# Performance work log

Hardware: AMD Instinct MI355X
Metric: run time of the kernel (lower is better)

Reference implementation:

```python
import jax, jax.numpy as jnp
import numpy as np

NUM_HEADS = 12


def setup_inputs() -> dict:
    key = jax.random.key(0)
    k1, k2, k3 = jax.random.split(key, 3)
    B, N, C = 2, 2048, 768
    x = jax.random.normal(k1, (B, N, C), dtype=jnp.float32)
    w_qkv = jax.random.normal(k2, (C, 3 * C), dtype=jnp.float32) * 0.02
    w_proj = jax.random.normal(k3, (C, C), dtype=jnp.float32) * 0.02
    b_proj = jnp.zeros((C,), dtype=jnp.float32)
    return {"x": x, "w_qkv": w_qkv, "w_proj": w_proj, "b_proj": b_proj}


def reference(x, w_qkv, w_proj, b_proj):
    B, N, C = x.shape
    H = NUM_HEADS
    D = C // H
    qkv = (x @ w_qkv).reshape(B, N, 3, H, D)  # [B,N,3,H,D]
    q = jnp.transpose(qkv[:, :, 0], (0, 2, 1, 3))  # [B,H,N,D]
    k = jnp.transpose(qkv[:, :, 1], (0, 2, 1, 3))
    v = jnp.transpose(qkv[:, :, 2], (0, 2, 1, 3))
    # ELU+1 feature map (note: self.scale is unused in the original forward)
    q = jax.nn.elu(q) + 1.0
    k = jax.nn.elu(k) + 1.0
    attn = jnp.einsum("bhnd,bhmd->bhnm", q, k)  # explicit O(N^2) as in source
    attn = attn / jnp.sum(attn, axis=-1, keepdims=True)
    out = jnp.einsum("bhnm,bhmd->bhnd", attn, v)  # [B,H,N,D]
    out = jnp.transpose(out, (0, 2, 1, 3)).reshape(B, N, C)
    out = out @ w_proj + b_proj
    return out, attn
```

## Files before the change

### kernel.cpp

```cpp
#include <hip/hip_runtime.h>
#include <hip/hip_bf16.h>
#include <cstdint>
#include <cmath>

#define BDIM 256

constexpr int Bb = 2;
constexpr int Nn = 2048;
constexpr int Cc = 768;
constexpr int Hh = 12;
constexpr int Dd = 64;
constexpr int TC = 3 * Cc;
constexpr int BH = Bb * Hh;
constexpr int NCHUNK = 16;
constexpr int CHROWS = Nn / NCHUNK;

typedef __attribute__((ext_vector_type(8))) short short8v;
typedef __attribute__((ext_vector_type(4))) float f32x4;

__device__ __forceinline__ float elu1(float x) {
  return x > 0.f ? x + 1.f : expf(x);
}

__device__ __forceinline__ unsigned short f2bf(float f) {
  uint32_t u = __float_as_uint(f);
  uint32_t r = (u + 0x7fff + ((u >> 16) & 1)) >> 16;
  return (unsigned short)r;
}
__device__ __forceinline__ float bf2f(unsigned short h) {
  return __uint_as_float(((uint32_t)h) << 16);
}

__device__ __forceinline__ void gll16(const unsigned short* g, unsigned short* ldsbase) {
  __builtin_amdgcn_global_load_lds((const __attribute__((address_space(1))) void*)g,
                                   (__attribute__((address_space(3))) void*)ldsbase,
                                   16, 0, 0);
}

constexpr int XBLK = 3072;
constexpr int WQBLK = (TC / 32) * (Cc / 32);
constexpr int WPBLK = (Cc / 32) * (Cc / 32);

__device__ __forceinline__ void castT_tile(const float* __restrict__ W,
                                           unsigned short* __restrict__ Wh,
                                           int K, int N, int n0, int k0, int tid,
                                           float (*t)[33]) {
  const int r = tid >> 3, c4 = (tid & 7) * 4;
  float4 v = *(const float4*)&W[(size_t)(k0 + r) * N + n0 + c4];
  t[r][c4 + 0] = v.x;
  t[r][c4 + 1] = v.y;
  t[r][c4 + 2] = v.z;
  t[r][c4 + 3] = v.w;
  __syncthreads();
  const int n = tid >> 3, k4 = (tid & 7) * 4;
  ushort4 h;
  h.x = f2bf(t[k4 + 0][n]);
  h.y = f2bf(t[k4 + 1][n]);
  h.z = f2bf(t[k4 + 2][n]);
  h.w = f2bf(t[k4 + 3][n]);
  *(ushort4*)&Wh[(size_t)(n0 + n) * K + k0 + k4] = h;
}

__global__ __launch_bounds__(BDIM) void fused_cast(const float* __restrict__ x,
                                                   const float* __restrict__ w_qkv,
                                                   const float* __restrict__ w_proj,
                                                   unsigned short* __restrict__ xh,
                                                   unsigned short* __restrict__ wqh,
                                                   unsigned short* __restrict__ wph) {
  __shared__ float t[32][33];
  const int bid = blockIdx.x, tid = threadIdx.x;
  if (bid < XBLK) {
    int i = (bid * BDIM + tid) * 4;
    float4 v = *(const float4*)&x[i];
    ushort4 h;
    h.x = f2bf(v.x);
    h.y = f2bf(v.y);
    h.z = f2bf(v.z);
    h.w = f2bf(v.w);
    *(ushort4*)&xh[i] = h;
  } else if (bid < XBLK + WQBLK) {
    int q = bid - XBLK;
    castT_tile(w_qkv, wqh, Cc, TC, (q % (TC / 32)) * 32, (q / (TC / 32)) * 32, tid, t);
  } else {
    int p = bid - XBLK - WQBLK;
    castT_tile(w_proj, wph, Cc, Cc, (p % (Cc / 32)) * 32, (p / (Cc / 32)) * 32, tid, t);
  }
}

template <int EP>
__device__ __forceinline__ void mfma_core(
    int bx, int by, int bz,
    const unsigned short* __restrict__ A, const unsigned short* __restrict__ Bt,
    const float* __restrict__ bias, const float* __restrict__ denom,
    float* __restrict__ C, int Mrows, int Nw, int K,
    long sAz, long sBz, long sCz,
    unsigned short* __restrict__ qpb, unsigned short* __restrict__ kpb,
    unsigned short* __restrict__ vpb,
    unsigned short* lds, float* dnls) {
  const unsigned short* A0 = A + (size_t)bz * sAz;
  const unsigned short* B0 = Bt + (size_t)bz * sBz;
  float* Cz = C + (size_t)bz * sCz;

  const int tid = threadIdx.x;
  const int wave = tid >> 6, lane = tid & 63;
  const int wr = wave >> 1, wc = wave & 1;
  const int row0 = by * 128, col0 = bx * 128;
  const int l15 = lane & 15, l4 = lane >> 4;
  const int srow = wave * 16 + (lane >> 2);
  const int scol = (lane & 3) * 8;
  const int wbase = wave * 512;

  float dnv_reg = 0.f;
  if constexpr (EP == 1) dnv_reg = denom[(size_t)bz * Mrows + row0 + (tid & 127)];

  auto STAGE = [&](int buf, int k0) {
    unsigned short* dst = lds + buf * 8192 + wbase;
    gll16(&A0[(size_t)(row0 + srow) * K + k0 + scol], dst);
    gll16(&A0[(size_t)(row0 + 64 + srow) * K + k0 + scol], dst + 2048);
    gll16(&B0[(size_t)(col0 + srow) * K + k0 + scol], dst + 4096);
    gll16(&B0[(size_t)(col0 + 64 + srow) * K + k0 + scol], dst + 6144);
  };

  f32x4 acc[4][4];
#pragma unroll
  for (int i = 0; i < 4; ++i)
#pragma unroll
    for (int j = 0; j < 4; ++j) acc[i][j] = {0.f, 0.f, 0.f, 0.f};

  auto COMPUTE = [&](int buf) {
    const unsigned short* la = lds + buf * 8192;
    const unsigned short* lb = la + 4096;
    short8v av[4], bv[4];
#pragma unroll
    for (int i = 0; i < 4; ++i)
      av[i] = *(const short8v*)&la[(wr * 64 + i * 16 + l15) * 32 + l4 * 8];
#pragma unroll
    for (int j = 0; j < 4; ++j)
      bv[j] = *(const short8v*)&lb[(wc * 64 + j * 16 + l15) * 32 + l4 * 8];
#pragma unroll
    for (int i = 0; i < 4; ++i)
#pragma unroll
      for (int j = 0; j < 4; ++j)
        acc[i][j] = __builtin_amdgcn_mfma_f32_16x16x32_bf16(av[i], bv[j], acc[i][j], 0, 0, 0);
  };

  const int nt = K >> 5;
  STAGE(0, 0);
  if (nt > 1) STAGE(1, 32);
  int cur = 0;
  for (int t = 0; t < nt; ++t) {
    if (t < nt - 1)
      asm volatile("s_waitcnt vmcnt(4)" ::: "memory");
    else
      asm volatile("s_waitcnt vmcnt(0)" ::: "memory");
    __builtin_amdgcn_s_barrier();
    COMPUTE(cur);
    if (t < nt - 2) {
      __builtin_amdgcn_s_barrier();
      STAGE(cur, (t + 2) * 32);
    }
    cur ^= 1;
  }

  if constexpr (EP == 0) {
#pragma unroll
    for (int i = 0; i < 4; ++i) {
      const int rbase = row0 + wr * 64 + i * 16 + l4 * 4;
#pragma unroll
      for (int j = 0; j < 4; ++j) {
        const int col = col0 + wc * 64 + j * 16 + l15;
        float bs = bias[col];
#pragma unroll
        for (int r = 0; r < 4; ++r)
          __builtin_nontemporal_store(acc[i][j][r] + bs,
                                      &Cz[(size_t)(rbase + r) * Nw + col]);
      }
    }
  } else if constexpr (EP == 1) {
    if (tid < 128) dnls[tid] = 1.0f / dnv_reg;
    float* fl = (float*)lds;
#pragma unroll
    for (int i = 0; i < 4; ++i) {
      __syncthreads();
#pragma unroll
      for (int j = 0; j < 4; ++j)
#pragma unroll
        for (int r = 0; r < 4; ++r)
          fl[(wr * 16 + l4 * 4 + r) * 132 + wc * 64 + j * 16 + l15] =
              acc[i][j][r] * dnls[wr * 64 + i * 16 + l4 * 4 + r];
      __syncthreads();
#pragma unroll
      for (int p = 0; p < 4; ++p) {
        int f4 = p * 256 + tid;
        int cr = f4 >> 5, c4 = (f4 & 31) * 4;
        f32x4 v = *(const f32x4*)&fl[cr * 132 + c4];
        int grow = row0 + (cr >> 4) * 64 + i * 16 + (cr & 15);
        __builtin_nontemporal_store(v, (f32x4*)&Cz[(size_t)grow * Nw + col0 + c4]);
      }
    }
  } else {
    const int tt = bx / 6;
    const int rcbase = (bx % 6) * 128 + wc * 64;
#pragma unroll
    for (int i = 0; i < 4; ++i) {
      const int rowb = row0 + wr * 64 + i * 16 + l4 * 4;
#pragma unroll
      for (int j = 0; j < 4; ++j) {
        const int rc = rcbase + j * 16 + l15;
        const int h = rc >> 6, d = rc & 63;
#pragma unroll
        for (int r = 0; r < 4; ++r) {
          const int row = rowb + r;
          const int b = row >> 11, n = row & (Nn - 1);
          const size_t idx = ((size_t)(b * Hh + h) * Nn + n) * 64 + d;
          float val = acc[i][j][r];
          if (tt == 0) {
            qpb[idx] = f2bf(elu1(val));
          } else if (tt == 1) {
            kpb[idx] = f2bf(elu1(val));
          } else {
            vpb[idx] = f2bf(val);
          }
        }
      }
    }
  }
}

__global__ __launch_bounds__(BDIM) void gemm_qkv_k(
    const unsigned short* __restrict__ xh, const unsigned short* __restrict__ wqh,
    unsigned short* __restrict__ qpb, unsigned short* __restrict__ kpb,
    unsigned short* __restrict__ vpb) {
  __shared__ __align__(16) unsigned short lds[16384];
  __shared__ float dnls[128];
  const int bid = blockIdx.x;
  const int swz = (bid & 7) * 72 + (bid >> 3);
  const int bx = swz % 18, by = swz / 18;
  mfma_core<2>(bx, by, 0, xh, wqh, nullptr, nullptr, nullptr, Bb * Nn, TC, Cc,
               0, 0, 0, qpb, kpb, vpb, lds, dnls);
}

__global__ __launch_bounds__(BDIM) void attn_proj_k(
    const unsigned short* __restrict__ qpb, const unsigned short* __restrict__ kpb,
    const float* __restrict__ denom, float* __restrict__ attn,
    const unsigned short* __restrict__ oph, const unsigned short* __restrict__ wph,
    const float* __restrict__ b_proj, float* __restrict__ out) {
  __shared__ __align__(16) unsigned short lds[16384];
  __shared__ float dnls[128];
  const int bid = blockIdx.x;
  if (bid < 6144) {
    const int swz = (bid & 7) * 768 + (bid >> 3);
    const int bz = swz >> 8, rem = swz & 255;
    const int by = rem >> 4, bx = rem & 15;
    mfma_core<1>(bx, by, bz, qpb, kpb, nullptr, denom, attn, Nn, Nn, Dd,
                 (long)Nn * Dd, (long)Nn * Dd, (long)Nn * Nn,
                 nullptr, nullptr, nullptr, lds, dnls);
  } else {
    const int p = bid - 6144;
    mfma_core<0>(p % 6, p / 6, 0, oph, wph, b_proj, nullptr, out, Bb * Nn, Cc, Cc,
                 0, 0, 0, nullptr, nullptr, nullptr, lds, dnls);
  }
}

__global__ __launch_bounds__(BDIM) void kv_partial(const unsigned short* __restrict__ kpb,
                                                   const unsigned short* __restrict__ vpb,
                                                   float* __restrict__ kvpart,
                                                   float* __restrict__ kspart) {
  const int chunk = blockIdx.x, bh = blockIdx.y;
  __shared__ unsigned short ks[16][64];
  __shared__ unsigned short vs[16][64];
  __shared__ float ksl[16][64];
  const int tid = threadIdx.x;
  const int e = tid & 63, dg = tid >> 6;
  const int srow = tid >> 4, sd4 = (tid & 15) * 4;
  float acc[16] = {};
  float ksp[4] = {0.f, 0.f, 0.f, 0.f};
  const int n0base = chunk * CHROWS;
  for (int s = 0; s < CHROWS; s += 16) {
    const int n = n0base + s + srow;
    ushort4 kk = *(const ushort4*)&kpb[((size_t)bh * Nn + n) * 64 + sd4];
    ushort4 vv = *(const ushort4*)&vpb[((size_t)bh * Nn + n) * 64 + sd4];
    __syncthreads();
    *(ushort4*)&ks[srow][sd4] = kk;
    *(ushort4*)&vs[srow][sd4] = vv;
    ksp[0] += bf2f(kk.x);
    ksp[1] += bf2f(kk.y);
    ksp[2] += bf2f(kk.z);
    ksp[3] += bf2f(kk.w);
    __syncthreads();
#pragma unroll
    for (int j = 0; j < 16; ++j) {
      const float v = bf2f(vs[j][e]);
      short8v k8a = *(const short8v*)&ks[j][dg * 16];
      short8v k8b = *(const short8v*)&ks[j][dg * 16 + 8];
#pragma unroll
      for (int d = 0; d < 8; ++d) acc[d] += bf2f((unsigned short)k8a[d]) * v;
#pragma unroll
      for (int d = 0; d < 8; ++d) acc[8 + d] += bf2f((unsigned short)k8b[d]) * v;
    }
  }
  float* outp = kvpart + (size_t)(bh * NCHUNK + chunk) * 4096;
#pragma unroll
  for (int d = 0; d < 16; ++d) outp[(dg * 16 + d) * 64 + e] = acc[d];
  ksl[srow][sd4 + 0] = ksp[0];
  ksl[srow][sd4 + 1] = ksp[1];
  ksl[srow][sd4 + 2] = ksp[2];
  ksl[srow][sd4 + 3] = ksp[3];
  __syncthreads();
  if (tid < 64) {
    float s2 = 0.f;
#pragma unroll
    for (int r = 0; r < 16; ++r) s2 += ksl[r][tid];
    kspart[(bh * NCHUNK + chunk) * 64 + tid] = s2;
  }
}

__global__ __launch_bounds__(BDIM) void kv_reduce(const float* __restrict__ kvpart,
                                                  const float* __restrict__ kspart,
                                                  unsigned short* __restrict__ kvtb,
                                                  float* __restrict__ ksum) {
  const int seg = blockIdx.x, bh = blockIdx.y, tid = threadIdx.x;
  const int idx = seg * 256 + tid;
  float s = 0.f;
#pragma unroll 4
  for (int c = 0; c < NCHUNK; ++c) s += kvpart[(size_t)(bh * NCHUNK + c) * 4096 + idx];
  const int dk = idx >> 6, dv = idx & 63;
  kvtb[(size_t)bh * 4096 + dv * 64 + dk] = f2bf(s);
  if (tid < 4) {
    int e = seg * 4 + tid;
    float s2 = 0.f;
#pragma unroll 4
    for (int c = 0; c < NCHUNK; ++c) s2 += kspart[(bh * NCHUNK + c) * 64 + e];
    ksum[bh * 64 + e] = s2;
  }
}

__global__ __launch_bounds__(BDIM) void outpre_mfma(
    const unsigned short* __restrict__ qpb, const unsigned short* __restrict__ kvtb,
    const float* __restrict__ ksum, float* __restrict__ denom,
    unsigned short* __restrict__ oph) {
  const int nc = blockIdx.x, bh = blockIdx.y;
  const int b = bh / Hh, h = bh % Hh;
  __shared__ float kss[64];
  __shared__ float dnls[128];
  const int tid = threadIdx.x;
  const int wv = tid >> 6, lane = tid & 63;
  const int l15 = lane & 15, l4 = lane >> 4;
  if (tid < 64) kss[tid] = ksum[bh * 64 + tid];

  const int rowb = nc * 128 + wv * 32;
  const unsigned short* Aq = qpb + ((size_t)bh * Nn + rowb) * 64;
  const unsigned short* Bk = kvtb + (size_t)bh * 4096;

  short8v av[2][2], bv[4][2];
#pragma unroll
  for (int ks = 0; ks < 2; ++ks) {
#pragma unroll
    for (int i = 0; i < 2; ++i)
      av[i][ks] = *(const short8v*)&Aq[(size_t)(i * 16 + l15) * 64 + ks * 32 + l4 * 8];
#pragma unroll
    for (int j = 0; j < 4; ++j)
      bv[j][ks] = *(const short8v*)&Bk[(size_t)(j * 16 + l15) * 64 + ks * 32 + l4 * 8];
  }
  f32x4 acc[2][4];
#pragma unroll
  for (int i = 0; i < 2; ++i)
#pragma unroll
    for (int j = 0; j < 4; ++j) acc[i][j] = {0.f, 0.f, 0.f, 0.f};
#pragma unroll
  for (int ks = 0; ks < 2; ++ks)
#pragma unroll
    for (int i = 0; i < 2; ++i)
#pragma unroll
      for (int j = 0; j < 4; ++j)
        acc[i][j] = __builtin_amdgcn_mfma_f32_16x16x32_bf16(av[i][ks], bv[j][ks],
                                                            acc[i][j], 0, 0, 0);

  __syncthreads();
  float dpart[2] = {0.f, 0.f};
#pragma unroll
  for (int ks = 0; ks < 2; ++ks)
#pragma unroll
    for (int i = 0; i < 2; ++i)
#pragma unroll
      for (int t = 0; t < 8; ++t)
        dpart[i] += bf2f((unsigned short)av[i][ks][t]) * kss[ks * 32 + l4 * 8 + t];
#pragma unroll
  for (int i = 0; i < 2; ++i) {
    dpart[i] += __shfl_xor(dpart[i], 16);
    dpart[i] += __shfl_xor(dpart[i], 32);
    if (l4 == 0) {
      dnls[wv * 32 + i * 16 + l15] = dpart[i];
      denom[(size_t)bh * Nn + rowb + i * 16 + l15] = dpart[i];
    }
  }
  __syncthreads();
#pragma unroll
  for (int i = 0; i < 2; ++i) {
#pragma unroll
    for (int r = 0; r < 4; ++r) {
      const int rl = i * 16 + l4 * 4 + r;
      const float rd = 1.0f / dnls[wv * 32 + rl];
      const int nrow = rowb + rl;
#pragma unroll
      for (int j = 0; j < 4; ++j)
        oph[((size_t)b * Nn + nrow) * Cc + h * 64 + j * 16 + l15] =
            f2bf(acc[i][j][r] * rd);
    }
  }
}

extern "C" void kernel_launch(void* const* d_in, const int* in_sizes, int n_in,
                              void* d_out, int out_size, void* d_ws, size_t ws_size,
                              hipStream_t stream) {
  const float* x = (const float*)d_in[0];
  const float* w_qkv = (const float*)d_in[1];
  const float* w_proj = (const float*)d_in[2];
  const float* b_proj = (const float*)d_in[3];
  float* out = (float*)d_out;
  float* attn = out + (size_t)Bb * Nn * Cc;

  float* ws = (float*)d_ws;
  float* kvpart = ws;
  float* kspart = kvpart + 1572864;
  float* ksum = kspart + 24576;
  float* denom = ksum + 2048;
  unsigned short* us = (unsigned short*)(denom + 49152);
  unsigned short* xh = us;
  unsigned short* wqh = xh + 3145728;
  unsigned short* qpb = wqh + 1769472;
  unsigned short* kpb = qpb + 3145728;
  unsigned short* vpb = kpb + 3145728;
  unsigned short* kvtb = vpb + 3145728;
  unsigned short* oph = kvtb + 98304;
  unsigned short* wph = oph + 3145728;

  fused_cast<<<dim3(XBLK + WQBLK + WPBLK), BDIM, 0, stream>>>(x, w_qkv, w_proj, xh, wqh,
                                                              wph);
  gemm_qkv_k<<<dim3(576), BDIM, 0, stream>>>(xh, wqh, qpb, kpb, vpb);
  kv_partial<<<dim3(NCHUNK, BH), BDIM, 0, stream>>>(kpb, vpb, kvpart, kspart);
  kv_reduce<<<dim3(16, BH), BDIM, 0, stream>>>(kvpart, kspart, kvtb, ksum);
  outpre_mfma<<<dim3(Nn / 128, BH), BDIM, 0, stream>>>(qpb, kvtb, ksum, denom, oph);
  attn_proj_k<<<dim3(6144 + 192), BDIM, 0, stream>>>(qpb, kpb, denom, attn,
                                                     oph, wph, b_proj, out);
}
```

Before: 149.7 us.

## Compute two attention column tiles per block with overlapped K prefetch

The attention-matrix kernel now computes a 128x256 output region per block as two 128-column tiles. It reuses the Q fragments held in registers and prefetches the second K tile while the first tile's epilogue writes out. The row denominator is recomputed in-kernel from ksum as a dot product with Q, so the denom array is no longer read. This halves the block count and cuts redundant Q loads, at the cost of more LDS per block and possibly lower occupancy.

```diff
diff --git a/kernel.cpp b/kernel.cpp
--- a/kernel.cpp
+++ b/kernel.cpp
@@ -91,12 +91,12 @@
 __device__ __forceinline__ void mfma_core(
     int bx, int by, int bz,
     const unsigned short* __restrict__ A, const unsigned short* __restrict__ Bt,
-    const float* __restrict__ bias, const float* __restrict__ denom,
+    const float* __restrict__ bias,
     float* __restrict__ C, int Mrows, int Nw, int K,
     long sAz, long sBz, long sCz,
     unsigned short* __restrict__ qpb, unsigned short* __restrict__ kpb,
     unsigned short* __restrict__ vpb,
-    unsigned short* lds, float* dnls) {
+    unsigned short* lds) {
   const unsigned short* A0 = A + (size_t)bz * sAz;
   const unsigned short* B0 = Bt + (size_t)bz * sBz;
   float* Cz = C + (size_t)bz * sCz;
@@ -109,9 +109,6 @@
   const int srow = wave * 16 + (lane >> 2);
   const int scol = (lane & 3) * 8;
   const int wbase = wave * 512;
-
-  float dnv_reg = 0.f;
-  if constexpr (EP == 1) dnv_reg = denom[(size_t)bz * Mrows + row0 + (tid & 127)];
 
   auto STAGE = [&](int buf, int k0) {
     unsigned short* dst = lds + buf * 8192 + wbase;
@@ -176,28 +173,6 @@
                                       &Cz[(size_t)(rbase + r) * Nw + col]);
       }
     }
-  } else if constexpr (EP == 1) {
-    if (tid < 128) dnls[tid] = 1.0f / dnv_reg;
-    float* fl = (float*)lds;
-#pragma unroll
-    for (int i = 0; i < 4; ++i) {
-      __syncthreads();
-#pragma unroll
-      for (int j = 0; j < 4; ++j)
-#pragma unroll
-        for (int r = 0; r < 4; ++r)
-          fl[(wr * 16 + l4 * 4 + r) * 132 + wc * 64 + j * 16 + l15] =
-              acc[i][j][r] * dnls[wr * 64 + i * 16 + l4 * 4 + r];
-      __syncthreads();
-#pragma unroll
-      for (int p = 0; p < 4; ++p) {
-        int f4 = p * 256 + tid;
-        int cr = f4 >> 5, c4 = (f4 & 31) * 4;
-        f32x4 v = *(const f32x4*)&fl[cr * 132 + c4];
-        int grow = row0 + (cr >> 4) * 64 + i * 16 + (cr & 15);
-        __builtin_nontemporal_store(v, (f32x4*)&Cz[(size_t)grow * Nw + col0 + c4]);
-      }
-    }
   } else {
     const int tt = bx / 6;
     const int rcbase = (bx % 6) * 128 + wc * 64;
@@ -232,34 +207,143 @@
     unsigned short* __restrict__ qpb, unsigned short* __restrict__ kpb,
     unsigned short* __restrict__ vpb) {
   __shared__ __align__(16) unsigned short lds[16384];
-  __shared__ float dnls[128];
   const int bid = blockIdx.x;
   const int swz = (bid & 7) * 72 + (bid >> 3);
   const int bx = swz % 18, by = swz / 18;
-  mfma_core<2>(bx, by, 0, xh, wqh, nullptr, nullptr, nullptr, Bb * Nn, TC, Cc,
-               0, 0, 0, qpb, kpb, vpb, lds, dnls);
+  mfma_core<2>(bx, by, 0, xh, wqh, nullptr, nullptr, Bb * Nn, TC, Cc,
+               0, 0, 0, qpb, kpb, vpb, lds);
 }
 
 __global__ __launch_bounds__(BDIM) void attn_proj_k(
     const unsigned short* __restrict__ qpb, const unsigned short* __restrict__ kpb,
-    const float* __restrict__ denom, float* __restrict__ attn,
+    const float* __restrict__ ksum, float* __restrict__ attn,
     const unsigned short* __restrict__ oph, const unsigned short* __restrict__ wph,
     const float* __restrict__ b_proj, float* __restrict__ out) {
-  __shared__ __align__(16) unsigned short lds[16384];
+  __shared__ __align__(16) unsigned short lds[24832];
+  __shared__ float kss[64];
   __shared__ float dnls[128];
-  const int bid = blockIdx.x;
-  if (bid < 6144) {
-    const int swz = (bid & 7) * 768 + (bid >> 3);
-    const int bz = swz >> 8, rem = swz & 255;
-    const int by = rem >> 4, bx = rem & 15;
-    mfma_core<1>(bx, by, bz, qpb, kpb, nullptr, denom, attn, Nn, Nn, Dd,
-                 (long)Nn * Dd, (long)Nn * Dd, (long)Nn * Nn,
-                 nullptr, nullptr, nullptr, lds, dnls);
-  } else {
-    const int p = bid - 6144;
-    mfma_core<0>(p % 6, p / 6, 0, oph, wph, b_proj, nullptr, out, Bb * Nn, Cc, Cc,
-                 0, 0, 0, nullptr, nullptr, nullptr, lds, dnls);
-  }
+  const int bid = blockIdx.x, tid = threadIdx.x;
+  if (bid >= 3072) {
+    const int p = bid - 3072;
+    mfma_core<0>(p % 6, p / 6, 0, oph, wph, b_proj, out, Bb * Nn, Cc, Cc,
+                 0, 0, 0, nullptr, nullptr, nullptr, lds);
+    return;
+  }
+  const int swz = (bid & 7) * 384 + (bid >> 3);
+  const int bz = swz >> 7, rem = swz & 127;
+  const int by = rem >> 3, bxp = rem & 7;
+  const int row0 = by * 128, col00 = bxp * 256;
+  const int wave = tid >> 6, lane = tid & 63;
+  const int wr = wave >> 1, wc = wave & 1;
+  const int l15 = lane & 15, l4 = lane >> 4;
+  const int srow = wave * 16 + (lane >> 2);
+  const int scol = (lane & 3) * 8;
+  const int wbase = wave * 512;
+  const unsigned short* Aq = qpb + (size_t)bz * Nn * 64;
+  const unsigned short* Bk = kpb + (size_t)bz * Nn * 64;
+  float* Cz = attn + (size_t)bz * Nn * Nn;
+  float* fl = (float*)(lds + 16384);
+
+  if (tid < 64) kss[tid] = ksum[bz * 64 + tid];
+
+  gll16(&Aq[(size_t)(row0 + srow) * 64 + scol], lds + wbase);
+  gll16(&Aq[(size_t)(row0 + 64 + srow) * 64 + scol], lds + 2048 + wbase);
+  gll16(&Aq[(size_t)(row0 + srow) * 64 + 32 + scol], lds + 4096 + wbase);
+  gll16(&Aq[(size_t)(row0 + 64 + srow) * 64 + 32 + scol], lds + 4096 + 2048 + wbase);
+  gll16(&Bk[(size_t)(col00 + srow) * 64 + scol], lds + 8192 + wbase);
+  gll16(&Bk[(size_t)(col00 + 64 + srow) * 64 + scol], lds + 8192 + 2048 + wbase);
+  gll16(&Bk[(size_t)(col00 + srow) * 64 + 32 + scol], lds + 12288 + wbase);
+  gll16(&Bk[(size_t)(col00 + 64 + srow) * 64 + 32 + scol], lds + 12288 + 2048 + wbase);
+
+  asm volatile("s_waitcnt vmcnt(0) lgkmcnt(0)" ::: "memory");
+  __builtin_amdgcn_s_barrier();
+
+  short8v av[2][4];
+#pragma unroll
+  for (int ks = 0; ks < 2; ++ks)
+#pragma unroll
+    for (int i = 0; i < 4; ++i)
+      av[ks][i] = *(const short8v*)&lds[ks * 4096 + (wr * 64 + i * 16 + l15) * 32 + l4 * 8];
+
+  float dp[4] = {0.f, 0.f, 0.f, 0.f};
+#pragma unroll
+  for (int ks = 0; ks < 2; ++ks)
+#pragma unroll
+    for (int i = 0; i < 4; ++i)
+#pragma unroll
+      for (int t = 0; t < 8; ++t)
+        dp[i] += bf2f((unsigned short)av[ks][i][t]) * kss[ks * 32 + l4 * 8 + t];
+#pragma unroll
+  for (int i = 0; i < 4; ++i) {
+    dp[i] += __shfl_xor(dp[i], 16);
+    dp[i] += __shfl_xor(dp[i], 32);
+    if (wc == 0 && l4 == 0) dnls[wr * 64 + i * 16 + l15] = 1.0f / dp[i];
+  }
+
+  f32x4 acc[4][4];
+  const unsigned short* lb = lds + 8192;
+
+  auto COMPUTE_T = [&]() {
+#pragma unroll
+    for (int i = 0; i < 4; ++i)
+#pragma unroll
+      for (int j = 0; j < 4; ++j) acc[i][j] = {0.f, 0.f, 0.f, 0.f};
+#pragma unroll
+    for (int ks = 0; ks < 2; ++ks) {
+      short8v bv[4];
+#pragma unroll
+      for (int j = 0; j < 4; ++j)
+        bv[j] = *(const short8v*)&lb[ks * 4096 + (wc * 64 + j * 16 + l15) * 32 + l4 * 8];
+#pragma unroll
+      for (int i = 0; i < 4; ++i)
+#pragma unroll
+        for (int j = 0; j < 4; ++j)
+          acc[i][j] = __builtin_amdgcn_mfma_f32_16x16x32_bf16(av[ks][i], bv[j],
+                                                              acc[i][j], 0, 0, 0);
+    }
+  };
+
+  auto EPILOGUE_T = [&](int colt) {
+#pragma unroll
+    for (int i = 0; i < 4; ++i) {
+      asm volatile("s_waitcnt lgkmcnt(0)" ::: "memory");
+      __builtin_amdgcn_s_barrier();
+#pragma unroll
+      for (int j = 0; j < 4; ++j)
+#pragma unroll
+        for (int r = 0; r < 4; ++r)
+          fl[(wr * 16 + l4 * 4 + r) * 132 + wc * 64 + j * 16 + l15] =
+              acc[i][j][r] * dnls[wr * 64 + i * 16 + l4 * 4 + r];
+      asm volatile("s_waitcnt lgkmcnt(0)" ::: "memory");
+      __builtin_amdgcn_s_barrier();
+#pragma unroll
+      for (int p = 0; p < 4; ++p) {
+        int f4 = p * 256 + tid;
+        int cr = f4 >> 5, c4 = (f4 & 31) * 4;
+        f32x4 v = *(const f32x4*)&fl[cr * 132 + c4];
+        int grow = row0 + (cr >> 4) * 64 + i * 16 + (cr & 15);
+        __builtin_nontemporal_store(v, (f32x4*)&Cz[(size_t)grow * Nn + colt + c4]);
+      }
+    }
+  };
+
+  COMPUTE_T();
+  asm volatile("s_waitcnt lgkmcnt(0)" ::: "memory");
+  __builtin_amdgcn_s_barrier();
+
+  const int col01 = col00 + 128;
+  gll16(&Bk[(size_t)(col01 + srow) * 64 + scol], lds + 8192 + wbase);
+  gll16(&Bk[(size_t)(col01 + 64 + srow) * 64 + scol], lds + 8192 + 2048 + wbase);
+  gll16(&Bk[(size_t)(col01 + srow) * 64 + 32 + scol], lds + 12288 + wbase);
+  gll16(&Bk[(size_t)(col01 + 64 + srow) * 64 + 32 + scol], lds + 12288 + 2048 + wbase);
+
+  EPILOGUE_T(col00);
+
+  asm volatile("s_waitcnt vmcnt(16) lgkmcnt(0)" ::: "memory");
+  __builtin_amdgcn_s_barrier();
+
+  COMPUTE_T();
+  EPILOGUE_T(col01);
 }
 
 __global__ __launch_bounds__(BDIM) void kv_partial(const unsigned short* __restrict__ kpb,
@@ -441,6 +525,6 @@
   kv_partial<<<dim3(NCHUNK, BH), BDIM, 0, stream>>>(kpb, vpb, kvpart, kspart);
   kv_reduce<<<dim3(16, BH), BDIM, 0, stream>>>(kvpart, kspart, kvtb, ksum);
   outpre_mfma<<<dim3(Nn / 128, BH), BDIM, 0, stream>>>(qpb, kvtb, ksum, denom, oph);
-  attn_proj_k<<<dim3(6144 + 192), BDIM, 0, stream>>>(qpb, kpb, denom, attn,
+  attn_proj_k<<<dim3(3072 + 192), BDIM, 0, stream>>>(qpb, kpb, ksum, attn,
                                                      oph, wph, b_proj, out);
 }
```

Result: no change. 151.8 us (+1.4%).
